# Kernel tuning notes

Measured on AMD Instinct MI355X. Metric: run time of the kernel, lower is better.

Reference implementation:

```python
import jax, jax.numpy as jnp
import numpy as np

B = 262144
NUM_CLASSES = 1000
K = 4
CODE_DIM = 256


def setup_inputs() -> dict:
    key = jax.random.key(0)
    k1, k2, k3 = jax.random.split(key, 3)
    codes = jax.random.uniform(k1, (B, CODE_DIM), dtype=jnp.float32)
    pred_class = jax.random.randint(k2, (B,), 0, NUM_CLASSES, dtype=jnp.int64)
    centroids = jax.random.uniform(k3, (NUM_CLASSES, K, CODE_DIM), dtype=jnp.float32)
    return {"codes": codes, "pred_class": pred_class, "centroids": centroids}


def reference(codes, pred_class, centroids):
    # Gather the k centroids of each sample's predicted class: [B, K, D]
    cents = centroids[pred_class]
    # Mean absolute (normalized Hamming-style) distance per centroid: [B, K]
    d = jnp.mean(jnp.abs(codes[:, None, :] - cents), axis=2)
    # Min over the k centroids -> [B]
    return jnp.min(d, axis=1)
```

## Files before the change

### kernel.cpp

```cpp
#include <hip/hip_runtime.h>


#define B_TOTAL     262144
#define NUM_CLASSES 1000
#define KC          4
#define DIM         256

typedef float    vf4 __attribute__((ext_vector_type(4)));
typedef _Float16 vh4 __attribute__((ext_vector_type(4)));

__global__ __launch_bounds__(256) void convert_kernel(
    const float* __restrict__ cent_f32, _Float16* __restrict__ cent_f16)
{
    const int i = blockIdx.x * 256 + threadIdx.x;
    const int n = NUM_CLASSES * KC * DIM / 4;
    if (i < n) {
        const vf4 v = ((const vf4*)cent_f32)[i];
        vh4 h;
        h.x = (_Float16)v.x; h.y = (_Float16)v.y;
        h.z = (_Float16)v.z; h.w = (_Float16)v.w;
        ((vh4*)cent_f16)[i] = h;
    }
}

__global__ __launch_bounds__(256) void sparse_codebook_h(
    const float*    __restrict__ codes,
    const int*      __restrict__ pred_class,
    const _Float16* __restrict__ cent_f16,
    float*          __restrict__ out)
{
    const int wave = (blockIdx.x * 256 + threadIdx.x) >> 6;
    const int lane = threadIdx.x & 63;
    const int q    = lane >> 4;
    const int l    = lane & 15;
    const int s0   = wave * 4;
    if (s0 >= B_TOTAL) return;

    const int my_sample = s0 + q;
    const int cls = pred_class[my_sample];

    const vf4* crow = (const vf4*)codes + (size_t)my_sample * 64;
    vf4 c[4];
#pragma unroll
    for (int j = 0; j < 4; ++j)
        c[j] = __builtin_nontemporal_load(&crow[j * 16 + l]);

    const vh4* cbase = (const vh4*)cent_f16 + (size_t)cls * (KC * DIM / 4);

    float s[KC];
#pragma unroll
    for (int k = 0; k < KC; ++k) {
        float acc = 0.0f;
#pragma unroll
        for (int j = 0; j < 4; ++j) {
            const vh4 g = cbase[k * 64 + j * 16 + l];
            acc += fabsf(c[j].x - (float)g.x) + fabsf(c[j].y - (float)g.y)
                 + fabsf(c[j].z - (float)g.z) + fabsf(c[j].w - (float)g.w);
        }
        s[k] = acc;
    }

#pragma unroll
    for (int off = 8; off >= 1; off >>= 1) {
#pragma unroll
        for (int k = 0; k < KC; ++k)
            s[k] += __shfl_xor(s[k], off, 64);
    }

    if (l == 0) {
        const float m = fminf(fminf(s[0], s[1]), fminf(s[2], s[3]));
        __builtin_nontemporal_store(m * (1.0f / (float)DIM), &out[my_sample]);
    }
}

extern "C" void kernel_launch(void* const* d_in, const int* in_sizes, int n_in,
                              void* d_out, int out_size, void* d_ws, size_t ws_size,
                              hipStream_t stream) {
    const float* codes = (const float*)d_in[0];
    const int*   pred  = (const int*)d_in[1];
    const float* cents = (const float*)d_in[2];
    float*       out   = (float*)d_out;
    _Float16*    tab   = (_Float16*)d_ws;

    const int nvec = NUM_CLASSES * KC * DIM / 4;
    convert_kernel<<<(nvec + 255) / 256, 256, 0, stream>>>(cents, tab);

    const int grid = (B_TOTAL * 16) / 256;
    sparse_codebook_h<<<grid, 256, 0, stream>>>(codes, pred, tab, out);
}
```

Before: 362.0 us.

## Use persistent grid with software-pipelined prefetch of next sample codes

Replaces the one-wave-per-4-samples launch with a fixed grid of 2048 blocks where each wave loops over several sample groups. While computing distances for the current group, it loads the class index and code row for the next group, to hide global memory latency and reduce block launch overhead. In exchange each wave holds more registers for the prefetched data, which can lower occupancy, and the fixed grid may underuse the GPU's parallelism for latency hiding.

```diff
diff --git a/kernel.cpp b/kernel.cpp
--- a/kernel.cpp
+++ b/kernel.cpp
@@ -5,6 +5,11 @@
 #define NUM_CLASSES 1000
 #define KC          4
 #define DIM         256
+
+#define NBLK        2048
+#define WAVES_TOT   (NBLK * 256 / 64)
+#define P_TOTAL     (B_TOTAL / 4)
+#define ITERS       (P_TOTAL / WAVES_TOT)
 
 typedef float    vf4 __attribute__((ext_vector_type(4)));
 typedef _Float16 vh4 __attribute__((ext_vector_type(4)));
@@ -23,7 +28,7 @@
     }
 }
 
-__global__ __launch_bounds__(256) void sparse_codebook_h(
+__global__ __launch_bounds__(256) void sparse_codebook_pipe(
     const float*    __restrict__ codes,
     const int*      __restrict__ pred_class,
     const _Float16* __restrict__ cent_f16,
@@ -33,43 +38,59 @@
     const int lane = threadIdx.x & 63;
     const int q    = lane >> 4;
     const int l    = lane & 15;
-    const int s0   = wave * 4;
-    if (s0 >= B_TOTAL) return;
 
-    const int my_sample = s0 + q;
-    const int cls = pred_class[my_sample];
+    int p = wave;
 
-    const vf4* crow = (const vf4*)codes + (size_t)my_sample * 64;
-    vf4 c[4];
+    int cls_cur = pred_class[p * 4 + q];
+    const vf4* crow = (const vf4*)codes + (size_t)(p * 4 + q) * 64;
+    vf4 c_cur[4];
 #pragma unroll
     for (int j = 0; j < 4; ++j)
-        c[j] = __builtin_nontemporal_load(&crow[j * 16 + l]);
+        c_cur[j] = __builtin_nontemporal_load(&crow[j * 16 + l]);
 
-    const vh4* cbase = (const vh4*)cent_f16 + (size_t)cls * (KC * DIM / 4);
+    for (int it = 0; it < ITERS; ++it) {
+        const int pn = p + WAVES_TOT;
+        int cls_nxt = 0;
+        vf4 c_nxt[4];
+        if (it + 1 < ITERS) {
+            cls_nxt = pred_class[pn * 4 + q];
+            const vf4* nrow = (const vf4*)codes + (size_t)(pn * 4 + q) * 64;
+#pragma unroll
+            for (int j = 0; j < 4; ++j)
+                c_nxt[j] = __builtin_nontemporal_load(&nrow[j * 16 + l]);
+        }
 
-    float s[KC];
+        const vh4* cbase = (const vh4*)cent_f16 + (size_t)cls_cur * (KC * DIM / 4);
+        float s[KC];
 #pragma unroll
-    for (int k = 0; k < KC; ++k) {
-        float acc = 0.0f;
+        for (int k = 0; k < KC; ++k) {
+            float acc = 0.0f;
 #pragma unroll
-        for (int j = 0; j < 4; ++j) {
-            const vh4 g = cbase[k * 64 + j * 16 + l];
-            acc += fabsf(c[j].x - (float)g.x) + fabsf(c[j].y - (float)g.y)
-                 + fabsf(c[j].z - (float)g.z) + fabsf(c[j].w - (float)g.w);
+            for (int j = 0; j < 4; ++j) {
+                const vh4 g = cbase[k * 64 + j * 16 + l];
+                acc += fabsf(c_cur[0 + j].x - (float)g.x)
+                     + fabsf(c_cur[0 + j].y - (float)g.y)
+                     + fabsf(c_cur[0 + j].z - (float)g.z)
+                     + fabsf(c_cur[0 + j].w - (float)g.w);
+            }
+            s[k] = acc;
         }
-        s[k] = acc;
-    }
 
 #pragma unroll
-    for (int off = 8; off >= 1; off >>= 1) {
+        for (int off = 8; off >= 1; off >>= 1)
 #pragma unroll
-        for (int k = 0; k < KC; ++k)
-            s[k] += __shfl_xor(s[k], off, 64);
-    }
+            for (int k = 0; k < KC; ++k)
+                s[k] += __shfl_xor(s[k], off, 64);
 
-    if (l == 0) {
-        const float m = fminf(fminf(s[0], s[1]), fminf(s[2], s[3]));
-        __builtin_nontemporal_store(m * (1.0f / (float)DIM), &out[my_sample]);
+        if (l == 0) {
+            const float m = fminf(fminf(s[0], s[1]), fminf(s[2], s[3]));
+            __builtin_nontemporal_store(m * (1.0f / (float)DIM), &out[p * 4 + q]);
+        }
+
+        p = pn;
+        cls_cur = cls_nxt;
+#pragma unroll
+        for (int j = 0; j < 4; ++j) c_cur[j] = c_nxt[j];
     }
 }
 
@@ -85,6 +106,5 @@
     const int nvec = NUM_CLASSES * KC * DIM / 4;
     convert_kernel<<<(nvec + 255) / 256, 256, 0, stream>>>(cents, tab);
 
-    const int grid = (B_TOTAL * 16) / 256;
-    sparse_codebook_h<<<grid, 256, 0, stream>>>(codes, pred, tab, out);
+    sparse_codebook_pipe<<<NBLK, 256, 0, stream>>>(codes, pred, tab, out);
 }
```

Measured after the change: 364.0 us. No clear change (+0.6%).
